# Kernel optimization log

Hardware: AMD Instinct MI355X
Metric: run time of the kernel (lower is better)

Reference implementation:

```python
import jax, jax.numpy as jnp
import numpy as np

N = 131072   # number of profile points
S = 64       # n_samples (PSF samples per point)
D = H = W = 256


def setup_inputs() -> dict:
    key = jax.random.key(0)
    k1, k2, k3, k4, k5, k6 = jax.random.split(key, 6)
    x = jax.random.normal(k1, (1, 1, D, H, W), dtype=jnp.float32)
    # voxel-space coordinates (x, y, z) inside the volume
    sampleGrid = jax.random.uniform(k2, (N, 3), dtype=jnp.float32) * jnp.array(
        [W - 1, H - 1, D - 1], dtype=jnp.float32)
    # small axis-angle rotations + translations: [N, 1, 6]
    rot = jax.random.normal(k3, (N, 1, 3), dtype=jnp.float32) * 0.02
    trn = jax.random.normal(k4, (N, 1, 3), dtype=jnp.float32) * 2.0
    ax = jnp.concatenate([rot, trn], axis=-1)
    half = jax.random.uniform(k5, (N, 1, 3), minval=1.0, maxval=3.0, dtype=jnp.float32)
    bound = jnp.concatenate([-half, half], axis=1)  # [N, 2, 3]
    InvCovScaled = jnp.eye(3, dtype=jnp.float32) * 0.5
    # torch.randn(...) - 0.5 from the original forward, hoisted out for determinism
    xyz_psf = jax.random.normal(k6, (N, S, 3), dtype=jnp.float32) - 0.5
    return dict(x=x, sampleGrid=sampleGrid, ax=ax, bound=bound,
                InvCovScaled=InvCovScaled, xyz_psf=xyz_psf)


def _axisangle2mat(a):
    # a: [N, 6] -> [N, 3, 4] = [R | t] via Rodrigues
    v, t = a[:, :3], a[:, 3:]
    theta = jnp.linalg.norm(v, axis=-1, keepdims=True)          # [N,1]
    k = v / jnp.maximum(theta, 1e-12)                            # unit axis
    kx, ky, kz = k[:, 0], k[:, 1], k[:, 2]
    z = jnp.zeros_like(kx)
    K = jnp.stack([z, -kz, ky, kz, z, -kx, -ky, kx, z], axis=-1).reshape(-1, 3, 3)
    ct = jnp.cos(theta)[..., None]  # [N,1,1]
    st = jnp.sin(theta)[..., None]
    I = jnp.eye(3, dtype=a.dtype)
    R = I + st * K + (1.0 - ct) * jnp.matmul(K, K)
    return jnp.concatenate([R, t[..., None]], axis=-1)           # [N,3,4]


def _grid_sample_3d(vol, grid):
    # vol: [D,H,W]; grid: [M,3] normalized coords (x,y,z) in [-1,1]
    # matches F.grid_sample(mode='bilinear', padding_mode='zeros', align_corners=False)
    d, h, w = vol.shape
    sizes = jnp.array([w, h, d], dtype=vol.dtype)
    pix = ((grid + 1.0) * sizes - 1.0) * 0.5                     # unnormalize
    ix, iy, iz = pix[:, 0], pix[:, 1], pix[:, 2]
    x0 = jnp.floor(ix); y0 = jnp.floor(iy); z0 = jnp.floor(iz)
    fx = ix - x0; fy = iy - y0; fz = iz - z0
    x0 = x0.astype(jnp.int32); y0 = y0.astype(jnp.int32); z0 = z0.astype(jnp.int32)

    def gather(xi, yi, zi):
        valid = ((xi >= 0) & (xi < w) & (yi >= 0) & (yi < h) & (zi >= 0) & (zi < d))
        xc = jnp.clip(xi, 0, w - 1)
        yc = jnp.clip(yi, 0, h - 1)
        zc = jnp.clip(zi, 0, d - 1)
        return jnp.where(valid, vol[zc, yc, xc], jnp.zeros((), vol.dtype))

    out = jnp.zeros(grid.shape[0], dtype=vol.dtype)
    for dx in (0, 1):
        wx = fx if dx else (1.0 - fx)
        for dy in (0, 1):
            wy = fy if dy else (1.0 - fy)
            for dz in (0, 1):
                wz = fz if dz else (1.0 - fz)
                out = out + gather(x0 + dx, y0 + dy, z0 + dz) * (wx * wy * wz)
    return out


def reference(x, sampleGrid, ax, bound, InvCovScaled, xyz_psf):
    vol = x[0, 0]                                                # [D,H,W]
    size = jnp.array([x.shape[-1], x.shape[-2], x.shape[-3]], dtype=x.dtype)  # [W,H,D]

    # pose matrices [N,1,3,4]
    mat = _axisangle2mat(ax.reshape(-1, 6)).reshape(ax.shape[:-1] + (3, 4))
    R = mat[..., :3]                                             # [N,1,3,3]
    T = mat[..., 3]                                              # [N,1,3]
    # trans_first=True: p' = R @ (p + T)
    p = sampleGrid[:, None] + T                                  # [N,1,3]
    mat_sampleGrid = jnp.einsum('nkij,nkj->nki', R, p)           # [N,1,3]

    # PSF offsets: [N,S,3]
    bound_psf = xyz_psf * ((bound[:, 1, :] - bound[:, 0, :]) * 0.5)[:, None]
    psf = mat_sampleGrid + bound_psf                             # [N,S,3]

    grid = 2.0 * (psf / (size - 1.0) - 0.5)                      # normalize per-axis
    psf_x = _grid_sample_3d(vol, grid.reshape(-1, 3)).reshape(psf.shape[:-1])  # [N,S]

    center = bound_psf
    q = jnp.einsum('nsi,ij,nsj->ns', center, InvCovScaled, center)
    w = jnp.exp(-0.5 * q)                                        # [N,S]
    y = (psf_x * w).sum(-1) / w.sum(-1)                          # [N]
    return y
```

## Files before the change

kernel.cpp:

```cpp
#include <hip/hip_runtime.h>


#define VOL_N 256
#define S_PSF 64
#define NBUCKET 4096
#define TBL_ELEMS (1 << 24)
#define TBL_BYTES ((size_t)TBL_ELEMS * 8)

typedef float vf4 __attribute__((ext_vector_type(4)));
typedef _Float16 vh4 __attribute__((ext_vector_type(4)));
typedef _Float16 vh8 __attribute__((ext_vector_type(8)));


__device__ __forceinline__ int bucket_of(const float* __restrict__ sg, int n) {
    int cx = min(max((int)sg[n * 3 + 0], 0), VOL_N - 1) >> 4;
    int cy = min(max((int)sg[n * 3 + 1], 0), VOL_N - 1) >> 4;
    int cz = min(max((int)sg[n * 3 + 2], 0), VOL_N - 1) >> 4;
    int m = 0;
    #pragma unroll
    for (int b = 0; b < 4; b++) {
        m |= (((cx >> b) & 1) << (3 * b))
           | (((cy >> b) & 1) << (3 * b + 1))
           | (((cz >> b) & 1) << (3 * b + 2));
    }
    return m;
}

__global__ void zero_hist_kernel(int* __restrict__ ws) {
    int i = blockIdx.x * blockDim.x + threadIdx.x;
    if (i < NBUCKET) ws[i] = 0;
}

__global__ void hist_kernel(const float* __restrict__ sg, int* __restrict__ ws, int N) {
    int n = blockIdx.x * blockDim.x + threadIdx.x;
    if (n >= N) return;
    atomicAdd(&ws[bucket_of(sg, n)], 1);
}

__global__ __launch_bounds__(1024) void scan_kernel(int* __restrict__ ws) {
    __shared__ int tmp[1024];
    const int t = threadIdx.x;
    int h0 = ws[t * 4 + 0], h1 = ws[t * 4 + 1], h2 = ws[t * 4 + 2], h3 = ws[t * 4 + 3];
    int s = h0 + h1 + h2 + h3;
    tmp[t] = s;
    __syncthreads();
    for (int off = 1; off < 1024; off <<= 1) {
        int v = (t >= off) ? tmp[t - off] : 0;
        __syncthreads();
        tmp[t] += v;
        __syncthreads();
    }
    int excl = tmp[t] - s;
    ws[NBUCKET + t * 4 + 0] = excl;
    ws[NBUCKET + t * 4 + 1] = excl + h0;
    ws[NBUCKET + t * 4 + 2] = excl + h0 + h1;
    ws[NBUCKET + t * 4 + 3] = excl + h0 + h1 + h2;
}

__global__ void scatter_kernel(const float* __restrict__ sg,
                               const float* __restrict__ ax,
                               const float* __restrict__ bound,
                               int* __restrict__ ws,
                               float* __restrict__ pre, int N) {
    int n = blockIdx.x * blockDim.x + threadIdx.x;
    if (n >= N) return;
    int b = bucket_of(sg, n);
    int pos = atomicAdd(&ws[NBUCKET + b], 1);
    ws[2 * NBUCKET + pos] = n;

    const float vx = ax[n * 6 + 0], vy = ax[n * 6 + 1], vz = ax[n * 6 + 2];
    const float tx = ax[n * 6 + 3], ty = ax[n * 6 + 4], tz = ax[n * 6 + 5];

    const float theta = sqrtf(vx * vx + vy * vy + vz * vz);
    const float kinv = 1.0f / fmaxf(theta, 1e-12f);
    const float kx = vx * kinv, ky = vy * kinv, kz = vz * kinv;
    const float ct = __cosf(theta), st = __sinf(theta);
    const float oc = 1.0f - ct;

    const float r00 = 1.0f + oc * (-(ky * ky + kz * kz));
    const float r01 = -st * kz + oc * kx * ky;
    const float r02 =  st * ky + oc * kx * kz;
    const float r10 =  st * kz + oc * kx * ky;
    const float r11 = 1.0f + oc * (-(kx * kx + kz * kz));
    const float r12 = -st * kx + oc * ky * kz;
    const float r20 = -st * ky + oc * kx * kz;
    const float r21 =  st * kx + oc * ky * kz;
    const float r22 = 1.0f + oc * (-(kx * kx + ky * ky));

    const float px = sg[n * 3 + 0] + tx;
    const float py = sg[n * 3 + 1] + ty;
    const float pz = sg[n * 3 + 2] + tz;

    const float cx = r00 * px + r01 * py + r02 * pz;
    const float cy = r10 * px + r11 * py + r12 * pz;
    const float cz = r20 * px + r21 * py + r22 * pz;

    const float hx = (bound[n * 6 + 3] - bound[n * 6 + 0]) * 0.5f;
    const float hy = (bound[n * 6 + 4] - bound[n * 6 + 1]) * 0.5f;
    const float hz = (bound[n * 6 + 5] - bound[n * 6 + 2]) * 0.5f;

    const float scale = (float)VOL_N / (float)(VOL_N - 1);
    float4 A = make_float4(cx * scale - 0.5f, cy * scale - 0.5f,
                           cz * scale - 0.5f, hx);
    float4 B = make_float4(hy, hz, 0.0f, 0.0f);
    *(float4*)(pre + (size_t)pos * 8)     = A;
    *(float4*)(pre + (size_t)pos * 8 + 4) = B;
}

__global__ __launch_bounds__(256) void build_quad_kernel(
    const float* __restrict__ vol, vh4* __restrict__ tbl) {
    const int t = blockIdx.x * 256 + threadIdx.x;
    const int x2 = (t & 127) << 1;
    const int y = (t >> 7) & 255;
    const int z = t >> 15;
    const float* r0 = vol + (z << 16) + (y << 8);
    const float* r1 = vol + (z << 16) + (min(y + 1, VOL_N - 1) << 8);
    const float2 a = *(const float2*)(r0 + x2);
    const float2 b = *(const float2*)(r1 + x2);
    const float a2 = (x2 == VOL_N - 2) ? a.y : r0[x2 + 2];
    const float b2 = (x2 == VOL_N - 2) ? b.y : r1[x2 + 2];

    union { vh8 h; vf4 f; } o;
    o.h = (vh8){(_Float16)a.x, (_Float16)a.y, (_Float16)b.x, (_Float16)b.y,
                (_Float16)a.y, (_Float16)a2,  (_Float16)b.y, (_Float16)b2};
    *(vf4*)(tbl + ((z << 16) + (y << 8) + x2)) = o.f;
}

template <bool USE_TBL>
__global__ __launch_bounds__(256, 4) void psf_sample_g4_kernel(
    const float* __restrict__ vol,
    const vh4* __restrict__ tbl,
    const float* __restrict__ invcov,
    const float* __restrict__ xyz_psf,
    const int* __restrict__ perm,
    const float* __restrict__ pre,
    float* __restrict__ out,
    int N)
{
    const int lane = threadIdx.x & 63;
    const int g = lane >> 4;
    const int t = lane & 15;

    int bid = blockIdx.x;
    const int nb = gridDim.x;
    if ((nb & 7) == 0) bid = (bid & 7) * (nb >> 3) + (bid >> 3);

    const int wave = threadIdx.x >> 6;
    const int i = (bid * 4 + wave) * 4 + g;
    const bool valid = i < N;
    const int ic = valid ? i : 0;
    const int n = perm[ic];

    const float4 A = *(const float4*)(pre + (size_t)ic * 8);
    const float4 B = *(const float4*)(pre + (size_t)ic * 8 + 4);
    const float icx = A.x, icy = A.y, icz = A.z;
    const float hx = A.w, hy = B.x, hz = B.y;

    const float m00 = invcov[0], m01 = invcov[1], m02 = invcov[2];
    const float m10 = invcov[3], m11 = invcov[4], m12 = invcov[5];
    const float m20 = invcov[6], m21 = invcov[7], m22 = invcov[8];

    const float* pp = xyz_psf + ((size_t)n * (S_PSF * 3) + t * 12);
    const vf4 f0 = __builtin_nontemporal_load((const vf4*)pp);
    const vf4 f1 = __builtin_nontemporal_load((const vf4*)pp + 1);
    const vf4 f2 = __builtin_nontemporal_load((const vf4*)pp + 2);

    const float gxx[4] = {f0.x, f0.w, f1.z, f2.y};
    const float gyy[4] = {f0.y, f1.x, f1.w, f2.z};
    const float gzz[4] = {f0.z, f1.y, f2.x, f2.w};

    const float scale = (float)VOL_N / (float)(VOL_N - 1);
    float num = 0.0f, den = 0.0f;

    #pragma unroll
    for (int k = 0; k < 4; ++k) {
        const float ox = gxx[k] * hx, oy = gyy[k] * hy, oz = gzz[k] * hz;

        const float ix = fmaf(ox, scale, icx);
        const float iy = fmaf(oy, scale, icy);
        const float iz = fmaf(oz, scale, icz);

        const float x0f = floorf(ix), y0f = floorf(iy), z0f = floorf(iz);
        const float fx = ix - x0f, fy = iy - y0f, fz = iz - z0f;
        const int x0 = (int)x0f, y0 = (int)y0f, z0 = (int)z0f;

        const float wx0 = ((unsigned)x0       < (unsigned)VOL_N) ? (1.0f - fx) : 0.0f;
        const float wx1 = ((unsigned)(x0 + 1) < (unsigned)VOL_N) ? fx          : 0.0f;
        const float wy0 = ((unsigned)y0       < (unsigned)VOL_N) ? (1.0f - fy) : 0.0f;
        const float wy1 = ((unsigned)(y0 + 1) < (unsigned)VOL_N) ? fy          : 0.0f;
        const float wz0 = ((unsigned)z0       < (unsigned)VOL_N) ? (1.0f - fz) : 0.0f;
        const float wz1 = ((unsigned)(z0 + 1) < (unsigned)VOL_N) ? fz          : 0.0f;

        float v000, v001, v010, v011, v100, v101, v110, v111;
        if (USE_TBL) {
            const int xg = min(max(x0, 0), VOL_N - 1);
            const int yg = min(max(y0, 0), VOL_N - 1);
            const int zg0 = min(max(z0, 0), VOL_N - 1);
            const int zg1 = min(max(z0 + 1, 0), VOL_N - 1);
            const int common = (yg << 8) + xg;
            const vh4 p0 = tbl[(zg0 << 16) + common];
            const vh4 p1 = tbl[(zg1 << 16) + common];
            const bool lox = x0 < 0;
            const bool loy = y0 < 0;
            float s00 = p0.x, s01 = p0.y, s10 = p0.z, s11 = p0.w;
            float a01 = lox ? s00 : s01, a11 = lox ? s10 : s11;
            v000 = s00;                 v001 = a01;
            v010 = loy ? s00 : s10;     v011 = loy ? a01 : a11;
            s00 = p1.x; s01 = p1.y; s10 = p1.z; s11 = p1.w;
            a01 = lox ? s00 : s01; a11 = lox ? s10 : s11;
            v100 = s00;                 v101 = a01;
            v110 = loy ? s00 : s10;     v111 = loy ? a01 : a11;
        } else {
            const int xc0 = min(max(x0, 0), VOL_N - 1);
            const int xc1 = min(max(x0 + 1, 0), VOL_N - 1);
            const int yc0 = min(max(y0, 0), VOL_N - 1);
            const int yc1 = min(max(y0 + 1, 0), VOL_N - 1);
            const int zc0 = min(max(z0, 0), VOL_N - 1);
            const int zc1 = min(max(z0 + 1, 0), VOL_N - 1);
            const int zo0 = zc0 << 16, zo1 = zc1 << 16;
            const int yo0 = yc0 << 8, yo1 = yc1 << 8;
            v000 = vol[zo0 + yo0 + xc0];
            v001 = vol[zo0 + yo0 + xc1];
            v010 = vol[zo0 + yo1 + xc0];
            v011 = vol[zo0 + yo1 + xc1];
            v100 = vol[zo1 + yo0 + xc0];
            v101 = vol[zo1 + yo0 + xc1];
            v110 = vol[zo1 + yo1 + xc0];
            v111 = vol[zo1 + yo1 + xc1];
        }

        const float r0 = fmaf(v001, wx1, v000 * wx0);
        const float r1 = fmaf(v011, wx1, v010 * wx0);
        const float r2 = fmaf(v101, wx1, v100 * wx0);
        const float r3 = fmaf(v111, wx1, v110 * wx0);
        const float s0 = fmaf(r1, wy1, r0 * wy0);
        const float s1 = fmaf(r3, wy1, r2 * wy0);
        const float acc = fmaf(s1, wz1, s0 * wz0);

        const float qx = fmaf(m00, ox, fmaf(m01, oy, m02 * oz));
        const float qy = fmaf(m10, ox, fmaf(m11, oy, m12 * oz));
        const float qz = fmaf(m20, ox, fmaf(m21, oy, m22 * oz));
        const float q = fmaf(ox, qx, fmaf(oy, qy, oz * qz));
        const float w = __expf(-0.5f * q);

        num = fmaf(acc, w, num);
        den += w;
    }

    #pragma unroll
    for (int m = 8; m >= 1; m >>= 1) {
        num += __shfl_xor(num, m, 64);
        den += __shfl_xor(den, m, 64);
    }
    if (t == 0 && valid) out[n] = num / den;
}

__global__ __launch_bounds__(256, 4) void psf_sample_plain_kernel(
    const float* __restrict__ vol,
    const float* __restrict__ sampleGrid,
    const float* __restrict__ ax,
    const float* __restrict__ bound,
    const float* __restrict__ invcov,
    const float* __restrict__ xyz_psf,
    float* __restrict__ out,
    int N)
{
    const int lane = threadIdx.x & 63;
    const int i = blockIdx.x * (blockDim.x >> 6) + (threadIdx.x >> 6);
    if (i >= N) return;
    const int n = __builtin_amdgcn_readfirstlane(i);

    const float vx = ax[n * 6 + 0], vy = ax[n * 6 + 1], vz = ax[n * 6 + 2];
    const float tx = ax[n * 6 + 3], ty = ax[n * 6 + 4], tz = ax[n * 6 + 5];
    const float theta = sqrtf(vx * vx + vy * vy + vz * vz);
    const float kinv = 1.0f / fmaxf(theta, 1e-12f);
    const float kx = vx * kinv, ky = vy * kinv, kz = vz * kinv;
    const float ct = __cosf(theta), st = __sinf(theta);
    const float oc = 1.0f - ct;
    const float r00 = 1.0f + oc * (-(ky * ky + kz * kz));
    const float r01 = -st * kz + oc * kx * ky;
    const float r02 =  st * ky + oc * kx * kz;
    const float r10 =  st * kz + oc * kx * ky;
    const float r11 = 1.0f + oc * (-(kx * kx + kz * kz));
    const float r12 = -st * kx + oc * ky * kz;
    const float r20 = -st * ky + oc * kx * kz;
    const float r21 =  st * kx + oc * ky * kz;
    const float r22 = 1.0f + oc * (-(kx * kx + ky * ky));
    const float px = sampleGrid[n * 3 + 0] + tx;
    const float py = sampleGrid[n * 3 + 1] + ty;
    const float pz = sampleGrid[n * 3 + 2] + tz;
    const float scale = (float)VOL_N / (float)(VOL_N - 1);
    const float icx = (r00 * px + r01 * py + r02 * pz) * scale - 0.5f;
    const float icy = (r10 * px + r11 * py + r12 * pz) * scale - 0.5f;
    const float icz = (r20 * px + r21 * py + r22 * pz) * scale - 0.5f;
    const float hx = (bound[n * 6 + 3] - bound[n * 6 + 0]) * 0.5f;
    const float hy = (bound[n * 6 + 4] - bound[n * 6 + 1]) * 0.5f;
    const float hz = (bound[n * 6 + 5] - bound[n * 6 + 2]) * 0.5f;

    const float m00 = invcov[0], m01 = invcov[1], m02 = invcov[2];
    const float m10 = invcov[3], m11 = invcov[4], m12 = invcov[5];
    const float m20 = invcov[6], m21 = invcov[7], m22 = invcov[8];

    const int pbase = (n * S_PSF + lane) * 3;
    const float ox = xyz_psf[pbase + 0] * hx;
    const float oy = xyz_psf[pbase + 1] * hy;
    const float oz = xyz_psf[pbase + 2] * hz;

    const float ix = fmaf(ox, scale, icx);
    const float iy = fmaf(oy, scale, icy);
    const float iz = fmaf(oz, scale, icz);
    const float x0f = floorf(ix), y0f = floorf(iy), z0f = floorf(iz);
    const float fx = ix - x0f, fy = iy - y0f, fz = iz - z0f;
    const int x0 = (int)x0f, y0 = (int)y0f, z0 = (int)z0f;

    const float wx0 = ((unsigned)x0       < (unsigned)VOL_N) ? (1.0f - fx) : 0.0f;
    const float wx1 = ((unsigned)(x0 + 1) < (unsigned)VOL_N) ? fx          : 0.0f;
    const float wy0 = ((unsigned)y0       < (unsigned)VOL_N) ? (1.0f - fy) : 0.0f;
    const float wy1 = ((unsigned)(y0 + 1) < (unsigned)VOL_N) ? fy          : 0.0f;
    const float wz0 = ((unsigned)z0       < (unsigned)VOL_N) ? (1.0f - fz) : 0.0f;
    const float wz1 = ((unsigned)(z0 + 1) < (unsigned)VOL_N) ? fz          : 0.0f;

    const int xc0 = min(max(x0, 0), VOL_N - 1);
    const int xc1 = min(max(x0 + 1, 0), VOL_N - 1);
    const int yc0 = min(max(y0, 0), VOL_N - 1);
    const int yc1 = min(max(y0 + 1, 0), VOL_N - 1);
    const int zc0 = min(max(z0, 0), VOL_N - 1);
    const int zc1 = min(max(z0 + 1, 0), VOL_N - 1);
    const int zo0 = zc0 << 16, zo1 = zc1 << 16;
    const int yo0 = yc0 << 8, yo1 = yc1 << 8;
    const float v000 = vol[zo0 + yo0 + xc0];
    const float v001 = vol[zo0 + yo0 + xc1];
    const float v010 = vol[zo0 + yo1 + xc0];
    const float v011 = vol[zo0 + yo1 + xc1];
    const float v100 = vol[zo1 + yo0 + xc0];
    const float v101 = vol[zo1 + yo0 + xc1];
    const float v110 = vol[zo1 + yo1 + xc0];
    const float v111 = vol[zo1 + yo1 + xc1];

    const float r0 = fmaf(v001, wx1, v000 * wx0);
    const float r1 = fmaf(v011, wx1, v010 * wx0);
    const float r2 = fmaf(v101, wx1, v100 * wx0);
    const float r3 = fmaf(v111, wx1, v110 * wx0);
    const float s0 = fmaf(r1, wy1, r0 * wy0);
    const float s1 = fmaf(r3, wy1, r2 * wy0);
    const float acc = fmaf(s1, wz1, s0 * wz0);

    const float qx = fmaf(m00, ox, fmaf(m01, oy, m02 * oz));
    const float qy = fmaf(m10, ox, fmaf(m11, oy, m12 * oz));
    const float qz = fmaf(m20, ox, fmaf(m21, oy, m22 * oz));
    const float q = fmaf(ox, qx, fmaf(oy, qy, oz * qz));
    const float w = __expf(-0.5f * q);

    float num = acc * w;
    float den = w;
    #pragma unroll
    for (int m = 32; m >= 1; m >>= 1) {
        num += __shfl_xor(num, m, 64);
        den += __shfl_xor(den, m, 64);
    }
    if (lane == 0) out[n] = num / den;
}

extern "C" void kernel_launch(void* const* d_in, const int* in_sizes, int n_in,
                              void* d_out, int out_size, void* d_ws, size_t ws_size,
                              hipStream_t stream) {
    const float* x        = (const float*)d_in[0];
    const float* sg       = (const float*)d_in[1];
    const float* ax       = (const float*)d_in[2];
    const float* bound    = (const float*)d_in[3];
    const float* invcov   = (const float*)d_in[4];
    const float* xyz_psf  = (const float*)d_in[5];
    float* out            = (float*)d_out;

    const int N = in_sizes[1] / 3;
    const size_t sort_bytes = (size_t)(2 * NBUCKET + N) * sizeof(int);
    const size_t sort_pad   = (sort_bytes + 31) & ~(size_t)31;
    const size_t pre_bytes  = (size_t)N * 8 * sizeof(float);

    const bool use_tbl  = ws_size >= TBL_BYTES + sort_pad + pre_bytes;
    const bool use_sort = use_tbl || ws_size >= sort_pad + pre_bytes;

    vh4* tbl = use_tbl ? (vh4*)d_ws : nullptr;
    char* base = (char*)d_ws + (use_tbl ? TBL_BYTES : 0);
    int* sort_ws = (int*)base;
    float* pre = (float*)(base + sort_pad);

    int* perm = nullptr;
    if (use_sort) {
        zero_hist_kernel<<<(NBUCKET + 255) / 256, 256, 0, stream>>>(sort_ws);
        hist_kernel<<<(N + 255) / 256, 256, 0, stream>>>(sg, sort_ws, N);
        scan_kernel<<<1, 1024, 0, stream>>>(sort_ws);
        scatter_kernel<<<(N + 255) / 256, 256, 0, stream>>>(sg, ax, bound, sort_ws, pre, N);
        perm = sort_ws + 2 * NBUCKET;
    }
    if (use_tbl) {
        build_quad_kernel<<<(VOL_N * VOL_N * VOL_N / 2) / 256, 256, 0, stream>>>(x, tbl);
    }

    if (use_sort) {
        dim3 block(256);
        dim3 grid((N + 15) / 16);
        if (use_tbl) {
            psf_sample_g4_kernel<true><<<grid, block, 0, stream>>>(
                x, tbl, invcov, xyz_psf, perm, pre, out, N);
        } else {
            psf_sample_g4_kernel<false><<<grid, block, 0, stream>>>(
                x, nullptr, invcov, xyz_psf, perm, pre, out, N);
        }
    } else {
        dim3 block(256);
        dim3 grid((N + 3) / 4);
        psf_sample_plain_kernel<<<grid, block, 0, stream>>>(
            x, sg, ax, bound, invcov, xyz_psf, out, N);
    }
}
```

Measured before the change: 339.9 us.

## Make sampling kernel persistent with per-wave chunks and software-prefetched point data

The g4 sampling kernel is replaced by a persistent kernel. Each wave walks a contiguous chunk of sorted points, one point per wave with one PSF sample per lane. The next point's perm index, precomputed pose and PSF offsets are loaded while the current point's table gathers are still in flight, so the gather latency should overlap with the global loads. The cost is a full 64-lane shuffle reduction per point and a serial dependency chain within each wave. Occupancy may drop if the 8-waves-per-SIMD launch bound is not met.

New measurement: 346.4 us. About the same (+1.9%).

```diff
diff --git a/kernel.cpp b/kernel.cpp
--- a/kernel.cpp
+++ b/kernel.cpp
@@ -127,7 +127,7 @@
 }
 
 template <bool USE_TBL>
-__global__ __launch_bounds__(256, 4) void psf_sample_g4_kernel(
+__global__ __launch_bounds__(256, 8) void psf_sample_pipe_kernel(
     const float* __restrict__ vol,
     const vh4* __restrict__ tbl,
     const float* __restrict__ invcov,
@@ -135,47 +135,44 @@
     const int* __restrict__ perm,
     const float* __restrict__ pre,
     float* __restrict__ out,
-    int N)
+    int N, int chunk)
 {
     const int lane = threadIdx.x & 63;
-    const int g = lane >> 4;
-    const int t = lane & 15;
 
     int bid = blockIdx.x;
     const int nb = gridDim.x;
     if ((nb & 7) == 0) bid = (bid & 7) * (nb >> 3) + (bid >> 3);
 
-    const int wave = threadIdx.x >> 6;
-    const int i = (bid * 4 + wave) * 4 + g;
-    const bool valid = i < N;
-    const int ic = valid ? i : 0;
-    const int n = perm[ic];
-
-    const float4 A = *(const float4*)(pre + (size_t)ic * 8);
-    const float4 B = *(const float4*)(pre + (size_t)ic * 8 + 4);
-    const float icx = A.x, icy = A.y, icz = A.z;
-    const float hx = A.w, hy = B.x, hz = B.y;
+    const int wid = __builtin_amdgcn_readfirstlane(
+        bid * (int)(blockDim.x >> 6) + (int)(threadIdx.x >> 6));
+    const int start = wid * chunk;
+    if (start >= N) return;
+    const int end = min(start + chunk, N);
 
     const float m00 = invcov[0], m01 = invcov[1], m02 = invcov[2];
     const float m10 = invcov[3], m11 = invcov[4], m12 = invcov[5];
     const float m20 = invcov[6], m21 = invcov[7], m22 = invcov[8];
-
-    const float* pp = xyz_psf + ((size_t)n * (S_PSF * 3) + t * 12);
-    const vf4 f0 = __builtin_nontemporal_load((const vf4*)pp);
-    const vf4 f1 = __builtin_nontemporal_load((const vf4*)pp + 1);
-    const vf4 f2 = __builtin_nontemporal_load((const vf4*)pp + 2);
-
-    const float gxx[4] = {f0.x, f0.w, f1.z, f2.y};
-    const float gyy[4] = {f0.y, f1.x, f1.w, f2.z};
-    const float gzz[4] = {f0.z, f1.y, f2.x, f2.w};
-
     const float scale = (float)VOL_N / (float)(VOL_N - 1);
-    float num = 0.0f, den = 0.0f;
-
-    #pragma unroll
-    for (int k = 0; k < 4; ++k) {
-        const float ox = gxx[k] * hx, oy = gyy[k] * hy, oz = gzz[k] * hz;
-
+
+    int n0 = perm[start];
+    float4 A0 = *(const float4*)(pre + (size_t)start * 8);
+    float4 B0 = *(const float4*)(pre + (size_t)start * 8 + 4);
+    const int i1c = min(start + 1, end - 1);
+    int n1 = perm[i1c];
+    float4 A1 = *(const float4*)(pre + (size_t)i1c * 8);
+    float4 B1 = *(const float4*)(pre + (size_t)i1c * 8 + 4);
+
+    const float* pp0 = xyz_psf + (size_t)n0 * (S_PSF * 3) + lane * 3;
+    float gx = __builtin_nontemporal_load(pp0 + 0);
+    float gy = __builtin_nontemporal_load(pp0 + 1);
+    float gz = __builtin_nontemporal_load(pp0 + 2);
+
+    for (int i = start; i < end; ++i) {
+        const int nout = n0;
+        const float icx = A0.x, icy = A0.y, icz = A0.z;
+        const float hx = A0.w, hy = B0.x, hz = B0.y;
+
+        const float ox = gx * hx, oy = gy * hy, oz = gz * hz;
         const float ix = fmaf(ox, scale, icx);
         const float iy = fmaf(oy, scale, icy);
         const float iz = fmaf(oz, scale, icz);
@@ -192,24 +189,18 @@
         const float wz1 = ((unsigned)(z0 + 1) < (unsigned)VOL_N) ? fz          : 0.0f;
 
         float v000, v001, v010, v011, v100, v101, v110, v111;
+        vh4 p0, p1;
+        bool lox = false, loy = false;
         if (USE_TBL) {
             const int xg = min(max(x0, 0), VOL_N - 1);
             const int yg = min(max(y0, 0), VOL_N - 1);
             const int zg0 = min(max(z0, 0), VOL_N - 1);
             const int zg1 = min(max(z0 + 1, 0), VOL_N - 1);
             const int common = (yg << 8) + xg;
-            const vh4 p0 = tbl[(zg0 << 16) + common];
-            const vh4 p1 = tbl[(zg1 << 16) + common];
-            const bool lox = x0 < 0;
-            const bool loy = y0 < 0;
-            float s00 = p0.x, s01 = p0.y, s10 = p0.z, s11 = p0.w;
-            float a01 = lox ? s00 : s01, a11 = lox ? s10 : s11;
-            v000 = s00;                 v001 = a01;
-            v010 = loy ? s00 : s10;     v011 = loy ? a01 : a11;
-            s00 = p1.x; s01 = p1.y; s10 = p1.z; s11 = p1.w;
-            a01 = lox ? s00 : s01; a11 = lox ? s10 : s11;
-            v100 = s00;                 v101 = a01;
-            v110 = loy ? s00 : s10;     v111 = loy ? a01 : a11;
+            p0 = tbl[(zg0 << 16) + common];
+            p1 = tbl[(zg1 << 16) + common];
+            lox = x0 < 0;
+            loy = y0 < 0;
         } else {
             const int xc0 = min(max(x0, 0), VOL_N - 1);
             const int xc1 = min(max(x0 + 1, 0), VOL_N - 1);
@@ -229,6 +220,28 @@
             v111 = vol[zo1 + yo1 + xc1];
         }
 
+        n0 = n1; A0 = A1; B0 = B1;
+        const int i2c = min(i + 2, end - 1);
+        n1 = perm[i2c];
+        A1 = *(const float4*)(pre + (size_t)i2c * 8);
+        B1 = *(const float4*)(pre + (size_t)i2c * 8 + 4);
+
+        const float* pp = xyz_psf + (size_t)n0 * (S_PSF * 3) + lane * 3;
+        const float gxn = __builtin_nontemporal_load(pp + 0);
+        const float gyn = __builtin_nontemporal_load(pp + 1);
+        const float gzn = __builtin_nontemporal_load(pp + 2);
+
+        if (USE_TBL) {
+            float s00 = p0.x, s01 = p0.y, s10 = p0.z, s11 = p0.w;
+            float a01 = lox ? s00 : s01, a11 = lox ? s10 : s11;
+            v000 = s00;                 v001 = a01;
+            v010 = loy ? s00 : s10;     v011 = loy ? a01 : a11;
+            s00 = p1.x; s01 = p1.y; s10 = p1.z; s11 = p1.w;
+            a01 = lox ? s00 : s01; a11 = lox ? s10 : s11;
+            v100 = s00;                 v101 = a01;
+            v110 = loy ? s00 : s10;     v111 = loy ? a01 : a11;
+        }
+
         const float r0 = fmaf(v001, wx1, v000 * wx0);
         const float r1 = fmaf(v011, wx1, v010 * wx0);
         const float r2 = fmaf(v101, wx1, v100 * wx0);
@@ -243,16 +256,17 @@
         const float q = fmaf(ox, qx, fmaf(oy, qy, oz * qz));
         const float w = __expf(-0.5f * q);
 
-        num = fmaf(acc, w, num);
-        den += w;
-    }
-
-    #pragma unroll
-    for (int m = 8; m >= 1; m >>= 1) {
-        num += __shfl_xor(num, m, 64);
-        den += __shfl_xor(den, m, 64);
-    }
-    if (t == 0 && valid) out[n] = num / den;
+        float num = acc * w;
+        float den = w;
+        #pragma unroll
+        for (int m = 32; m >= 1; m >>= 1) {
+            num += __shfl_xor(num, m, 64);
+            den += __shfl_xor(den, m, 64);
+        }
+        if (lane == 0) out[nout] = num / den;
+
+        gx = gxn; gy = gyn; gz = gzn;
+    }
 }
 
 __global__ __launch_bounds__(256, 4) void psf_sample_plain_kernel(
@@ -398,14 +412,16 @@
     }
 
     if (use_sort) {
+        const int nwaves = 8192;
+        const int chunk = (N + nwaves - 1) / nwaves;
         dim3 block(256);
-        dim3 grid((N + 15) / 16);
+        dim3 grid(2048);
         if (use_tbl) {
-            psf_sample_g4_kernel<true><<<grid, block, 0, stream>>>(
-                x, tbl, invcov, xyz_psf, perm, pre, out, N);
+            psf_sample_pipe_kernel<true><<<grid, block, 0, stream>>>(
+                x, tbl, invcov, xyz_psf, perm, pre, out, N, chunk);
         } else {
-            psf_sample_g4_kernel<false><<<grid, block, 0, stream>>>(
-                x, nullptr, invcov, xyz_psf, perm, pre, out, N);
+            psf_sample_pipe_kernel<false><<<grid, block, 0, stream>>>(
+                x, nullptr, invcov, xyz_psf, perm, pre, out, N, chunk);
         }
     } else {
         dim3 block(256);
```

## Drop fp16 quad gather table and sample fp32 volume with one wave per point

Applied to the files above, without the earlier changes.

Removes the pre-pass that built a 128MB fp16 neighbour-quad table and instead gathers eight fp32 voxels directly from the volume. The sampling kernel is restructured to one 64-lane wave per profile point with one PSF sample per lane and a full-wave shuffle reduction. This avoids the table-build read/write traffic and fp16 rounding, at the cost of more gather instructions per sample and less per-thread ILP.

After: 312.0 us. -8.2%, faster.

```diff
diff --git a/kernel.cpp b/kernel.cpp
--- a/kernel.cpp
+++ b/kernel.cpp
@@ -4,13 +4,6 @@
 #define VOL_N 256
 #define S_PSF 64
 #define NBUCKET 4096
-#define TBL_ELEMS (1 << 24)
-#define TBL_BYTES ((size_t)TBL_ELEMS * 8)
-
-typedef float vf4 __attribute__((ext_vector_type(4)));
-typedef _Float16 vh4 __attribute__((ext_vector_type(4)));
-typedef _Float16 vh8 __attribute__((ext_vector_type(8)));
-
 
 __device__ __forceinline__ int bucket_of(const float* __restrict__ sg, int n) {
     int cx = min(max((int)sg[n * 3 + 0], 0), VOL_N - 1) >> 4;
@@ -107,29 +100,8 @@
     *(float4*)(pre + (size_t)pos * 8 + 4) = B;
 }
 
-__global__ __launch_bounds__(256) void build_quad_kernel(
-    const float* __restrict__ vol, vh4* __restrict__ tbl) {
-    const int t = blockIdx.x * 256 + threadIdx.x;
-    const int x2 = (t & 127) << 1;
-    const int y = (t >> 7) & 255;
-    const int z = t >> 15;
-    const float* r0 = vol + (z << 16) + (y << 8);
-    const float* r1 = vol + (z << 16) + (min(y + 1, VOL_N - 1) << 8);
-    const float2 a = *(const float2*)(r0 + x2);
-    const float2 b = *(const float2*)(r1 + x2);
-    const float a2 = (x2 == VOL_N - 2) ? a.y : r0[x2 + 2];
-    const float b2 = (x2 == VOL_N - 2) ? b.y : r1[x2 + 2];
-
-    union { vh8 h; vf4 f; } o;
-    o.h = (vh8){(_Float16)a.x, (_Float16)a.y, (_Float16)b.x, (_Float16)b.y,
-                (_Float16)a.y, (_Float16)a2,  (_Float16)b.y, (_Float16)b2};
-    *(vf4*)(tbl + ((z << 16) + (y << 8) + x2)) = o.f;
-}
-
-template <bool USE_TBL>
-__global__ __launch_bounds__(256, 4) void psf_sample_g4_kernel(
+__global__ __launch_bounds__(256, 4) void psf_sample_vol_kernel(
     const float* __restrict__ vol,
-    const vh4* __restrict__ tbl,
     const float* __restrict__ invcov,
     const float* __restrict__ xyz_psf,
     const int* __restrict__ perm,
@@ -138,121 +110,86 @@
     int N)
 {
     const int lane = threadIdx.x & 63;
-    const int g = lane >> 4;
-    const int t = lane & 15;
 
     int bid = blockIdx.x;
     const int nb = gridDim.x;
     if ((nb & 7) == 0) bid = (bid & 7) * (nb >> 3) + (bid >> 3);
 
-    const int wave = threadIdx.x >> 6;
-    const int i = (bid * 4 + wave) * 4 + g;
-    const bool valid = i < N;
-    const int ic = valid ? i : 0;
-    const int n = perm[ic];
-
-    const float4 A = *(const float4*)(pre + (size_t)ic * 8);
-    const float4 B = *(const float4*)(pre + (size_t)ic * 8 + 4);
+    const int i = bid * (int)(blockDim.x >> 6) + (int)(threadIdx.x >> 6);
+    if (i >= N) return;
+    const int n = __builtin_amdgcn_readfirstlane(perm[i]);
+
+    const float4 A = *(const float4*)(pre + (size_t)i * 8);
+    const float4 B = *(const float4*)(pre + (size_t)i * 8 + 4);
     const float icx = A.x, icy = A.y, icz = A.z;
     const float hx = A.w, hy = B.x, hz = B.y;
 
     const float m00 = invcov[0], m01 = invcov[1], m02 = invcov[2];
     const float m10 = invcov[3], m11 = invcov[4], m12 = invcov[5];
     const float m20 = invcov[6], m21 = invcov[7], m22 = invcov[8];
-
-    const float* pp = xyz_psf + ((size_t)n * (S_PSF * 3) + t * 12);
-    const vf4 f0 = __builtin_nontemporal_load((const vf4*)pp);
-    const vf4 f1 = __builtin_nontemporal_load((const vf4*)pp + 1);
-    const vf4 f2 = __builtin_nontemporal_load((const vf4*)pp + 2);
-
-    const float gxx[4] = {f0.x, f0.w, f1.z, f2.y};
-    const float gyy[4] = {f0.y, f1.x, f1.w, f2.z};
-    const float gzz[4] = {f0.z, f1.y, f2.x, f2.w};
-
     const float scale = (float)VOL_N / (float)(VOL_N - 1);
-    float num = 0.0f, den = 0.0f;
-
+
+    const int pbase = (n * S_PSF + lane) * 3;
+    const float gx = xyz_psf[pbase + 0];
+    const float gy = xyz_psf[pbase + 1];
+    const float gz = xyz_psf[pbase + 2];
+    const float ox = gx * hx, oy = gy * hy, oz = gz * hz;
+
+    const float ix = fmaf(ox, scale, icx);
+    const float iy = fmaf(oy, scale, icy);
+    const float iz = fmaf(oz, scale, icz);
+
+    const float x0f = floorf(ix), y0f = floorf(iy), z0f = floorf(iz);
+    const float fx = ix - x0f, fy = iy - y0f, fz = iz - z0f;
+    const int x0 = (int)x0f, y0 = (int)y0f, z0 = (int)z0f;
+
+    const float wx0 = ((unsigned)x0       < (unsigned)VOL_N) ? (1.0f - fx) : 0.0f;
+    const float wx1 = ((unsigned)(x0 + 1) < (unsigned)VOL_N) ? fx          : 0.0f;
+    const float wy0 = ((unsigned)y0       < (unsigned)VOL_N) ? (1.0f - fy) : 0.0f;
+    const float wy1 = ((unsigned)(y0 + 1) < (unsigned)VOL_N) ? fy          : 0.0f;
+    const float wz0 = ((unsigned)z0       < (unsigned)VOL_N) ? (1.0f - fz) : 0.0f;
+    const float wz1 = ((unsigned)(z0 + 1) < (unsigned)VOL_N) ? fz          : 0.0f;
+
+    const int xc0 = min(max(x0, 0), VOL_N - 1);
+    const int xc1 = min(max(x0 + 1, 0), VOL_N - 1);
+    const int yc0 = min(max(y0, 0), VOL_N - 1);
+    const int yc1 = min(max(y0 + 1, 0), VOL_N - 1);
+    const int zc0 = min(max(z0, 0), VOL_N - 1);
+    const int zc1 = min(max(z0 + 1, 0), VOL_N - 1);
+    const int zo0 = zc0 << 16, zo1 = zc1 << 16;
+    const int yo0 = yc0 << 8, yo1 = yc1 << 8;
+
+    const float v000 = vol[zo0 + yo0 + xc0];
+    const float v001 = vol[zo0 + yo0 + xc1];
+    const float v010 = vol[zo0 + yo1 + xc0];
+    const float v011 = vol[zo0 + yo1 + xc1];
+    const float v100 = vol[zo1 + yo0 + xc0];
+    const float v101 = vol[zo1 + yo0 + xc1];
+    const float v110 = vol[zo1 + yo1 + xc0];
+    const float v111 = vol[zo1 + yo1 + xc1];
+
+    const float r0 = fmaf(v001, wx1, v000 * wx0);
+    const float r1 = fmaf(v011, wx1, v010 * wx0);
+    const float r2 = fmaf(v101, wx1, v100 * wx0);
+    const float r3 = fmaf(v111, wx1, v110 * wx0);
+    const float s0 = fmaf(r1, wy1, r0 * wy0);
+    const float s1 = fmaf(r3, wy1, r2 * wy0);
+    const float acc = fmaf(s1, wz1, s0 * wz0);
+
+    const float qx = fmaf(m00, ox, fmaf(m01, oy, m02 * oz));
+    const float qy = fmaf(m10, ox, fmaf(m11, oy, m12 * oz));
+    const float qz = fmaf(m20, ox, fmaf(m21, oy, m22 * oz));
+    const float q = fmaf(ox, qx, fmaf(oy, qy, oz * qz));
+    const float w = __expf(-0.5f * q);
+
+    float num = acc * w;
+    float den = w;
     #pragma unroll
-    for (int k = 0; k < 4; ++k) {
-        const float ox = gxx[k] * hx, oy = gyy[k] * hy, oz = gzz[k] * hz;
-
-        const float ix = fmaf(ox, scale, icx);
-        const float iy = fmaf(oy, scale, icy);
-        const float iz = fmaf(oz, scale, icz);
-
-        const float x0f = floorf(ix), y0f = floorf(iy), z0f = floorf(iz);
-        const float fx = ix - x0f, fy = iy - y0f, fz = iz - z0f;
-        const int x0 = (int)x0f, y0 = (int)y0f, z0 = (int)z0f;
-
-        const float wx0 = ((unsigned)x0       < (unsigned)VOL_N) ? (1.0f - fx) : 0.0f;
-        const float wx1 = ((unsigned)(x0 + 1) < (unsigned)VOL_N) ? fx          : 0.0f;
-        const float wy0 = ((unsigned)y0       < (unsigned)VOL_N) ? (1.0f - fy) : 0.0f;
-        const float wy1 = ((unsigned)(y0 + 1) < (unsigned)VOL_N) ? fy          : 0.0f;
-        const float wz0 = ((unsigned)z0       < (unsigned)VOL_N) ? (1.0f - fz) : 0.0f;
-        const float wz1 = ((unsigned)(z0 + 1) < (unsigned)VOL_N) ? fz          : 0.0f;
-
-        float v000, v001, v010, v011, v100, v101, v110, v111;
-        if (USE_TBL) {
-            const int xg = min(max(x0, 0), VOL_N - 1);
-            const int yg = min(max(y0, 0), VOL_N - 1);
-            const int zg0 = min(max(z0, 0), VOL_N - 1);
-            const int zg1 = min(max(z0 + 1, 0), VOL_N - 1);
-            const int common = (yg << 8) + xg;
-            const vh4 p0 = tbl[(zg0 << 16) + common];
-            const vh4 p1 = tbl[(zg1 << 16) + common];
-            const bool lox = x0 < 0;
-            const bool loy = y0 < 0;
-            float s00 = p0.x, s01 = p0.y, s10 = p0.z, s11 = p0.w;
-            float a01 = lox ? s00 : s01, a11 = lox ? s10 : s11;
-            v000 = s00;                 v001 = a01;
-            v010 = loy ? s00 : s10;     v011 = loy ? a01 : a11;
-            s00 = p1.x; s01 = p1.y; s10 = p1.z; s11 = p1.w;
-            a01 = lox ? s00 : s01; a11 = lox ? s10 : s11;
-            v100 = s00;                 v101 = a01;
-            v110 = loy ? s00 : s10;     v111 = loy ? a01 : a11;
-        } else {
-            const int xc0 = min(max(x0, 0), VOL_N - 1);
-            const int xc1 = min(max(x0 + 1, 0), VOL_N - 1);
-            const int yc0 = min(max(y0, 0), VOL_N - 1);
-            const int yc1 = min(max(y0 + 1, 0), VOL_N - 1);
-            const int zc0 = min(max(z0, 0), VOL_N - 1);
-            const int zc1 = min(max(z0 + 1, 0), VOL_N - 1);
-            const int zo0 = zc0 << 16, zo1 = zc1 << 16;
-            const int yo0 = yc0 << 8, yo1 = yc1 << 8;
-            v000 = vol[zo0 + yo0 + xc0];
-            v001 = vol[zo0 + yo0 + xc1];
-            v010 = vol[zo0 + yo1 + xc0];
-            v011 = vol[zo0 + yo1 + xc1];
-            v100 = vol[zo1 + yo0 + xc0];
-            v101 = vol[zo1 + yo0 + xc1];
-            v110 = vol[zo1 + yo1 + xc0];
-            v111 = vol[zo1 + yo1 + xc1];
-        }
-
-        const float r0 = fmaf(v001, wx1, v000 * wx0);
-        const float r1 = fmaf(v011, wx1, v010 * wx0);
-        const float r2 = fmaf(v101, wx1, v100 * wx0);
-        const float r3 = fmaf(v111, wx1, v110 * wx0);
-        const float s0 = fmaf(r1, wy1, r0 * wy0);
-        const float s1 = fmaf(r3, wy1, r2 * wy0);
-        const float acc = fmaf(s1, wz1, s0 * wz0);
-
-        const float qx = fmaf(m00, ox, fmaf(m01, oy, m02 * oz));
-        const float qy = fmaf(m10, ox, fmaf(m11, oy, m12 * oz));
-        const float qz = fmaf(m20, ox, fmaf(m21, oy, m22 * oz));
-        const float q = fmaf(ox, qx, fmaf(oy, qy, oz * qz));
-        const float w = __expf(-0.5f * q);
-
-        num = fmaf(acc, w, num);
-        den += w;
-    }
-
-    #pragma unroll
-    for (int m = 8; m >= 1; m >>= 1) {
+    for (int m = 32; m >= 1; m >>= 1) {
         num += __shfl_xor(num, m, 64);
         den += __shfl_xor(den, m, 64);
     }
-    if (t == 0 && valid) out[n] = num / den;
+    if (lane == 0) out[n] = num / den;
 }
 
 __global__ __launch_bounds__(256, 4) void psf_sample_plain_kernel(
@@ -377,36 +314,22 @@
     const size_t sort_pad   = (sort_bytes + 31) & ~(size_t)31;
     const size_t pre_bytes  = (size_t)N * 8 * sizeof(float);
 
-    const bool use_tbl  = ws_size >= TBL_BYTES + sort_pad + pre_bytes;
-    const bool use_sort = use_tbl || ws_size >= sort_pad + pre_bytes;
-
-    vh4* tbl = use_tbl ? (vh4*)d_ws : nullptr;
-    char* base = (char*)d_ws + (use_tbl ? TBL_BYTES : 0);
-    int* sort_ws = (int*)base;
-    float* pre = (float*)(base + sort_pad);
-
-    int* perm = nullptr;
+    const bool use_sort = ws_size >= sort_pad + pre_bytes;
+
     if (use_sort) {
+        int* sort_ws = (int*)d_ws;
+        float* pre = (float*)((char*)d_ws + sort_pad);
+        int* perm = sort_ws + 2 * NBUCKET;
+
         zero_hist_kernel<<<(NBUCKET + 255) / 256, 256, 0, stream>>>(sort_ws);
         hist_kernel<<<(N + 255) / 256, 256, 0, stream>>>(sg, sort_ws, N);
         scan_kernel<<<1, 1024, 0, stream>>>(sort_ws);
         scatter_kernel<<<(N + 255) / 256, 256, 0, stream>>>(sg, ax, bound, sort_ws, pre, N);
-        perm = sort_ws + 2 * NBUCKET;
-    }
-    if (use_tbl) {
-        build_quad_kernel<<<(VOL_N * VOL_N * VOL_N / 2) / 256, 256, 0, stream>>>(x, tbl);
-    }
-
-    if (use_sort) {
+
         dim3 block(256);
-        dim3 grid((N + 15) / 16);
-        if (use_tbl) {
-            psf_sample_g4_kernel<true><<<grid, block, 0, stream>>>(
-                x, tbl, invcov, xyz_psf, perm, pre, out, N);
-        } else {
-            psf_sample_g4_kernel<false><<<grid, block, 0, stream>>>(
-                x, nullptr, invcov, xyz_psf, perm, pre, out, N);
-        }
+        dim3 grid((N + 3) / 4);
+        psf_sample_vol_kernel<<<grid, block, 0, stream>>>(
+            x, invcov, xyz_psf, perm, pre, out, N);
     } else {
         dim3 block(256);
         dim3 grid((N + 3) / 4);
```
